# Kernel optimization log

Hardware: AMD Instinct MI355X
Metric: run time of the kernel (lower is better)

## Reference

```python
import jax, jax.numpy as jnp
from jax import lax
import numpy as np

KSIZE = 3
SOFTMAX_SCALE = 10.0
EPS = 1e-4  # escape_NaN in the original


def extract_patches(x, k):
    """x: [B,H,W,C] -> [B,H,W,k*k,C]; SAME zero padding, stride 1.
    Patch elements ordered (ky, kx) row-major, channels innermost, matching
    tf.image.extract_patches."""
    B, H, W, C = x.shape
    p = k // 2
    xp = jnp.pad(x, ((0, 0), (p, p), (p, p), (0, 0)))
    shifts = [xp[:, i:i + H, j:j + W, :] for i in range(k) for j in range(k)]
    return jnp.stack(shifts, axis=3)


def setup_inputs() -> dict:
    key = jax.random.key(0)
    k1, k2, k3 = jax.random.split(key, 3)
    B, H, W, C = 2, 64, 64, 128
    x1 = jax.random.normal(k1, (B, H, W, C), dtype=jnp.float32)
    x2 = jax.random.normal(k2, (B, H, W, C), dtype=jnp.float32)
    mask = jax.random.uniform(k3, (B, H, W, 1), dtype=jnp.float32)
    return {"x1": x1, "x2": x2, "mask": mask}


def reference(x1, x2, mask):
    # First call of the stateful layer: att_scores_prev is None, so the
    # mask-derived `mm` only updates internal state and does not affect y.
    # mask is already at x2's spatial size, so the bilinear resize is identity.
    B, H, W, C = x2.shape
    k = KSIZE
    L = H * W

    # Key patches from x2, L2-normalized per patch (the conv kernels).
    Pq = extract_patches(x2, k).reshape(B, L, k * k * C)  # [B, HW, k*k*C]
    norm = jnp.sqrt(jnp.sum(Pq * Pq, axis=-1, keepdims=True))
    Wn = Pq / jnp.maximum(norm, EPS)

    # conv2d(x2_i, wi_normed, SAME) == patches(x2_i) @ Wn_i^T  -> [B, HW, L]
    scores = jnp.einsum('bxq,blq->bxl', Pq, Wn).reshape(B, H, W, L)

    # tf.nn.avg_pool2d(., 3, 1, 'SAME') * 9 (TF excludes padding from count)
    sums = lax.reduce_window(scores, 0.0, lax.add, (1, 3, 3, 1), (1, 1, 1, 1), 'SAME')
    cnt = lax.reduce_window(jnp.ones((1, H, W, 1), scores.dtype), 0.0, lax.add,
                            (1, 3, 3, 1), (1, 1, 1, 1), 'SAME')
    pooled = sums / cnt * 9.0

    att = jax.nn.softmax(pooled * SOFTMAX_SCALE, axis=-1)  # [B, H, W, L]

    # Value patches from x1, arranged as conv kernels [k,k,C,L] per image.
    raw = extract_patches(x1, k).reshape(B, L, k, k, C).transpose(0, 2, 3, 4, 1)

    def tconv(a, kern):
        # tf.nn.conv2d_transpose(att, raw_wi, [1,H,W,C], strides=1, 'SAME')
        return lax.conv_transpose(a[None], kern, (1, 1), 'SAME',
                                  dimension_numbers=('NHWC', 'HWIO', 'NHWC'),
                                  transpose_kernel=True)[0]

    y = jax.vmap(tconv)(att, raw)  # [B, H, W, C]
    return y
```

## Files before the change

kernel.cpp:

```cpp
#include <hip/hip_runtime.h>
#include <hip/hip_bf16.h>
#include <math.h>


constexpr int Hh = 64;
constexpr int Ww = 64;
constexpr int CDIM = 128;
constexpr int LDIM = Hh * Ww;

typedef __attribute__((ext_vector_type(8))) short bf16x8;
typedef __attribute__((ext_vector_type(4))) float f32x4;
typedef __attribute__((ext_vector_type(4))) _Float16 f16x4;

__global__ __launch_bounds__(256)
void k_split(const float* __restrict__ X, __hip_bfloat16* __restrict__ Xh_,
             __hip_bfloat16* __restrict__ Xl_, size_t inStrideF, size_t wsStrideB) {
    const int z = blockIdx.z;
    const float* Xb = X + (size_t)z * inStrideF;
    __hip_bfloat16* Xh = (__hip_bfloat16*)((char*)Xh_ + (size_t)z * wsStrideB);
    __hip_bfloat16* Xl = (__hip_bfloat16*)((char*)Xl_ + (size_t)z * wsStrideB);
    const int i = (blockIdx.x * 256 + threadIdx.x) * 4;
    const float4 v = *(const float4*)(Xb + i);
    __hip_bfloat16 h[4], l[4];
    const float f[4] = {v.x, v.y, v.z, v.w};
    #pragma unroll
    for (int j = 0; j < 4; ++j) {
        h[j] = __float2bfloat16(f[j]);
        l[j] = __float2bfloat16(f[j] - __bfloat162float(h[j]));
    }
    *(ushort4*)(Xh + i) = *(ushort4*)h;
    *(ushort4*)(Xl + i) = *(ushort4*)l;
}

__global__ __launch_bounds__(256)
void k_pixnorm(const float* __restrict__ X2, float* __restrict__ pixn_,
               size_t inStrideF, size_t wsStrideB) {
    const int z = blockIdx.z;
    const float* Xb = X2 + (size_t)z * inStrideF;
    float* pixn = (float*)((char*)pixn_ + (size_t)z * wsStrideB);
    const int t = threadIdx.x;
    const int row = blockIdx.x * 64 + (t >> 2);
    const int seg = t & 3;
    const float* p = Xb + (size_t)row * CDIM + seg * 32;
    float s = 0.f;
    #pragma unroll
    for (int j = 0; j < 8; ++j) {
        const float4 v = *(const float4*)(p + 4 * j);
        s += v.x * v.x + v.y * v.y + v.z * v.z + v.w * v.w;
    }
    s += __shfl_xor(s, 1);
    s += __shfl_xor(s, 2);
    if (seg == 0) pixn[row] = s;
}

__global__ void k_invnorm(const float* __restrict__ pixn_, float* __restrict__ invn_,
                          size_t wsStrideB) {
    const int z = blockIdx.z;
    const float* pixn = (const float*)((const char*)pixn_ + (size_t)z * wsStrideB);
    float* invn = (float*)((char*)invn_ + (size_t)z * wsStrideB);
    const int l = blockIdx.x * 256 + threadIdx.x;
    const int ly = l >> 6, lx = l & 63;
    float s = 0.f;
    #pragma unroll
    for (int ty = -1; ty <= 1; ++ty)
        #pragma unroll
        for (int tx = -1; tx <= 1; ++tx) {
            if ((unsigned)(ly + ty) < 64u && (unsigned)(lx + tx) < 64u)
                s += pixn[l + ty * Ww + tx];
        }
    invn[l] = 1.0f / fmaxf(sqrtf(s), 1e-4f);
}

__global__ __launch_bounds__(256)
void k_gemm_d(const __hip_bfloat16* __restrict__ Xh_,
              const __hip_bfloat16* __restrict__ Xl_, _Float16* __restrict__ Ds_,
              size_t wsStrideB) {
    const int z = blockIdx.z;
    const __hip_bfloat16* Xh = (const __hip_bfloat16*)((const char*)Xh_ + (size_t)z * wsStrideB);
    const __hip_bfloat16* Xl = (const __hip_bfloat16*)((const char*)Xl_ + (size_t)z * wsStrideB);
    _Float16* Ds = (_Float16*)((char*)Ds_ + (size_t)z * wsStrideB);
    const int t = threadIdx.x;
    const int wave = t >> 6, lane = t & 63;
    const int quad = lane >> 4, l16 = lane & 15;
    const int bm = blockIdx.x * 128 + wave * 32;
    const int bn = blockIdx.y * 128;
    f32x4 acc[2][8] = {};
    for (int k0 = 0; k0 < CDIM; k0 += 32) {
        const int kq = k0 + quad * 8;
        bf16x8 ah[2], al[2], bh[8], bl[8];
        #pragma unroll
        for (int mi = 0; mi < 2; ++mi) {
            const size_t r = (size_t)(bm + mi * 16 + l16) * CDIM + kq;
            ah[mi] = *(const bf16x8*)(Xh + r);
            al[mi] = *(const bf16x8*)(Xl + r);
        }
        #pragma unroll
        for (int nf = 0; nf < 8; ++nf) {
            const size_t r = (size_t)(bn + nf * 16 + l16) * CDIM + kq;
            bh[nf] = *(const bf16x8*)(Xh + r);
            bl[nf] = *(const bf16x8*)(Xl + r);
        }
        #pragma unroll
        for (int mi = 0; mi < 2; ++mi)
            #pragma unroll
            for (int nf = 0; nf < 8; ++nf) {
                acc[mi][nf] = __builtin_amdgcn_mfma_f32_16x16x32_bf16(ah[mi], bh[nf], acc[mi][nf], 0, 0, 0);
                acc[mi][nf] = __builtin_amdgcn_mfma_f32_16x16x32_bf16(ah[mi], bl[nf], acc[mi][nf], 0, 0, 0);
                acc[mi][nf] = __builtin_amdgcn_mfma_f32_16x16x32_bf16(al[mi], bh[nf], acc[mi][nf], 0, 0, 0);
            }
    }
    #pragma unroll
    for (int mi = 0; mi < 2; ++mi)
        #pragma unroll
        for (int nf = 0; nf < 8; ++nf) {
            const int row = bm + mi * 16 + quad * 4;
            const int col = bn + nf * 16 + l16;
            #pragma unroll
            for (int r = 0; r < 4; ++r)
                Ds[(size_t)(row + r) * LDIM + ((col - row - r) & (LDIM - 1))] =
                    (_Float16)acc[mi][nf][r];
        }
}

__global__ __launch_bounds__(256)
void k_gdiag(const _Float16* __restrict__ Ds_, _Float16* __restrict__ G_,
             size_t wsStrideB) {
    const int z = blockIdx.z;
    const _Float16* Ds = (const _Float16*)((const char*)Ds_ + (size_t)z * wsStrideB);
    _Float16* G = (_Float16*)((char*)G_ + (size_t)z * wsStrideB);
    constexpr int T = 8;
    const int f = blockIdx.x + gridDim.x * blockIdx.y;
    const int swz = (f & 7) * 256 + (f >> 3);
    const int d0 = ((swz & 3) * 256 + threadIdx.x) * 4;
    const int x0 = (swz >> 2) * T;
    const int xyc = x0 >> 6;
    const int xxb = x0 & 63;
    float acc[T][4] = {};
    #pragma unroll
    for (int c = 0; c < 3; ++c) {
        const int bc = c * 64 - 65;
        const int ty = c - 1;
        if ((unsigned)(xyc + ty) >= 64u) continue;
        float w[T + 2][4];
        #pragma unroll
        for (int u = 0; u < T + 2; ++u) {
            const int r = x0 + bc + u;
            if ((unsigned)r < (unsigned)LDIM) {
                const f16x4 v = *(const f16x4*)(Ds + (size_t)r * LDIM + d0);
                w[u][0] = (float)v.x; w[u][1] = (float)v.y;
                w[u][2] = (float)v.z; w[u][3] = (float)v.w;
            } else {
                w[u][0] = w[u][1] = w[u][2] = w[u][3] = 0.f;
            }
        }
        #pragma unroll
        for (int i = 0; i < T; ++i) {
            const int px = xxb + i;
            const int p  = x0 + i;
            #pragma unroll
            for (int j = 0; j < 4; ++j) {
                const int l  = (p + d0 + j) & (LDIM - 1);
                const int ly = l >> 6, lx = l & 63;
                if ((unsigned)(ly + ty) < 64u) {
                    float s = acc[i][j];
                    if (px > 0 && lx > 0)   s += w[i][j];
                    s += w[i + 1][j];
                    if (px < 63 && lx < 63) s += w[i + 2][j];
                    acc[i][j] = s;
                }
            }
        }
    }
    #pragma unroll
    for (int i = 0; i < T; ++i) {
        const int x = x0 + i;
        const int l0i = (x + d0) & (LDIM - 1);
        union { _Float16 h[4]; unsigned short us[4]; unsigned int ui[2]; } cv;
        #pragma unroll
        for (int j = 0; j < 4; ++j) cv.h[j] = (_Float16)acc[i][j];
        unsigned short* bp = (unsigned short*)(G + (size_t)x * LDIM);
        if (l0i <= LDIM - 4) {
            if (!(l0i & 1)) {
                *(unsigned int*)(bp + l0i)     = cv.ui[0];
                *(unsigned int*)(bp + l0i + 2) = cv.ui[1];
            } else {
                bp[l0i] = cv.us[0];
                *(unsigned int*)(bp + l0i + 1) =
                    (unsigned int)cv.us[1] | ((unsigned int)cv.us[2] << 16);
                bp[l0i + 3] = cv.us[3];
            }
        } else {
            #pragma unroll
            for (int j = 0; j < 4; ++j)
                bp[(l0i + j) & (LDIM - 1)] = cv.us[j];
        }
    }
}

__global__ __launch_bounds__(256)
void k_pool_stats(const _Float16* __restrict__ G_, const float* __restrict__ invn_,
                  _Float16* __restrict__ Ps_, float* __restrict__ rowm_,
                  float* __restrict__ rowrz_, size_t wsStrideB) {
    const int z = blockIdx.z;
    const _Float16* G = (const _Float16*)((const char*)G_ + (size_t)z * wsStrideB);
    const float* invn = (const float*)((const char*)invn_ + (size_t)z * wsStrideB);
    _Float16* Ps = (_Float16*)((char*)Ps_ + (size_t)z * wsStrideB);
    float* rowm = (float*)((char*)rowm_ + (size_t)z * wsStrideB);
    float* rowrz = (float*)((char*)rowrz_ + (size_t)z * wsStrideB);
    constexpr int T = 8;
    const int f = blockIdx.x;
    const int swz = (f & 7) * 64 + (f >> 3);
    const int x0 = swz * T;
    const int t  = threadIdx.x;
    const int xyc = x0 >> 6;
    const int xxb = x0 & 63;
    const int cy = 1 + (xyc > 0) + (xyc < 63);
    float sc[T];
    #pragma unroll
    for (int i = 0; i < T; ++i) {
        const int xx = xxb + i;
        sc[i] = 90.0f / (float)(cy * (1 + (xx > 0) + (xx < 63)));
    }
    float m[T], Z[T];
    #pragma unroll
    for (int i = 0; i < T; ++i) { m[i] = -1e30f; Z[i] = 0.f; }

    for (int ch = 0; ch < 4; ++ch) {
        const int l0 = ch * 1024 + t * 4;
        const f32x4 inl = *(const f32x4*)(invn + l0);
        f32x4 acc[T];
        #pragma unroll
        for (int i = 0; i < T; ++i) acc[i] = (f32x4){0.f, 0.f, 0.f, 0.f};
        #pragma unroll
        for (int c = 0; c < 3; ++c) {
            const int bc = c * 64 - 65;
            const int ty = c - 1;
            if ((unsigned)(xyc + ty) >= 64u) continue;
            f32x4 w[T + 2];
            #pragma unroll
            for (int u = 0; u < T + 2; ++u) {
                const int r = x0 + bc + u;
                if ((unsigned)r < (unsigned)LDIM) {
                    const f16x4 v = *(const f16x4*)(G + (size_t)r * LDIM + l0);
                    w[u] = (f32x4){(float)v.x, (float)v.y, (float)v.z, (float)v.w};
                } else {
                    w[u] = (f32x4){0.f, 0.f, 0.f, 0.f};
                }
            }
            #pragma unroll
            for (int i = 0; i < T; ++i) {
                const int xx = xxb + i;
                if (xx > 0)  acc[i] += w[i];
                acc[i] += w[i + 1];
                if (xx < 63) acc[i] += w[i + 2];
            }
        }
        #pragma unroll
        for (int i = 0; i < T; ++i) {
            const f32x4 p = acc[i] * sc[i] * inl;
            const int x = x0 + i;
            const int c0 = (l0 - x) & (LDIM - 1);
            union { _Float16 h[4]; unsigned short us[4]; unsigned int ui[2]; } cv;
            float pr[4];
            #pragma unroll
            for (int j = 0; j < 4; ++j) {
                cv.h[j] = (_Float16)p[j];
                pr[j] = (float)cv.h[j];
            }
            unsigned short* bp = (unsigned short*)(Ps + (size_t)x * LDIM);
            if (c0 <= LDIM - 4) {
                if (!(c0 & 1)) {
                    *(unsigned int*)(bp + c0)     = cv.ui[0];
                    *(unsigned int*)(bp + c0 + 2) = cv.ui[1];
                } else {
                    bp[c0] = cv.us[0];
                    *(unsigned int*)(bp + c0 + 1) =
                        (unsigned int)cv.us[1] | ((unsigned int)cv.us[2] << 16);
                    bp[c0 + 3] = cv.us[3];
                }
            } else {
                #pragma unroll
                for (int j = 0; j < 4; ++j)
                    bp[(c0 + j) & (LDIM - 1)] = cv.us[j];
            }
            const float mx4 = fmaxf(fmaxf(pr[0], pr[1]), fmaxf(pr[2], pr[3]));
            const float nm = fmaxf(m[i], mx4);
            Z[i] = Z[i] * __expf(m[i] - nm)
                 + __expf(pr[0] - nm) + __expf(pr[1] - nm)
                 + __expf(pr[2] - nm) + __expf(pr[3] - nm);
            m[i] = nm;
        }
    }
    __shared__ float sm[256], sz[256];
    for (int i = 0; i < T; ++i) {
        __syncthreads();
        sm[t] = m[i]; sz[t] = Z[i];
        __syncthreads();
        for (int off = 128; off > 0; off >>= 1) {
            if (t < off) {
                const float m2 = sm[t + off], z2 = sz[t + off];
                const float nm = fmaxf(sm[t], m2);
                sz[t] = sz[t] * __expf(sm[t] - nm) + z2 * __expf(m2 - nm);
                sm[t] = nm;
            }
            __syncthreads();
        }
        if (t == 0) { rowm[x0 + i] = sm[0]; rowrz[x0 + i] = 1.0f / sz[0]; }
    }
}

__global__ __launch_bounds__(256)
void k_x1t(const float* __restrict__ X1, __hip_bfloat16* __restrict__ X1T_,
           size_t inStrideF, size_t wsStrideB) {
    const int z = blockIdx.z;
    const float* X1b = X1 + (size_t)z * inStrideF;
    __hip_bfloat16* X1T = (__hip_bfloat16*)((char*)X1T_ + (size_t)z * wsStrideB);
    __shared__ float tile[32][132];
    const int k0 = blockIdx.x * 32;
    const int t  = threadIdx.x;
    const int kr = t >> 3;
    const int c0 = (t & 7) * 16;
    #pragma unroll
    for (int j = 0; j < 4; ++j) {
        const float4 v = *(const float4*)(X1b + (size_t)(k0 + kr) * CDIM + c0 + 4 * j);
        tile[kr][c0 + 4 * j + 0] = v.x;
        tile[kr][c0 + 4 * j + 1] = v.y;
        tile[kr][c0 + 4 * j + 2] = v.z;
        tile[kr][c0 + 4 * j + 3] = v.w;
    }
    __syncthreads();
    const int c  = t >> 1;
    const int kh = (t & 1) * 16;
    __hip_bfloat16 outv[16];
    #pragma unroll
    for (int j = 0; j < 16; ++j)
        outv[j] = __float2bfloat16(tile[kh + j][c]);
    *(ushort4*)(X1T + (size_t)c * LDIM + k0 + kh)      = *(ushort4*)(outv);
    *(ushort4*)(X1T + (size_t)c * LDIM + k0 + kh + 4)  = *(ushort4*)(outv + 4);
    *(ushort4*)(X1T + (size_t)c * LDIM + k0 + kh + 8)  = *(ushort4*)(outv + 8);
    *(ushort4*)(X1T + (size_t)c * LDIM + k0 + kh + 12) = *(ushort4*)(outv + 12);
}

__global__ __launch_bounds__(256)
void k_att2(const _Float16* __restrict__ Ps_, const float* __restrict__ rowm_,
            const float* __restrict__ rowrz_, __hip_bfloat16* __restrict__ A2_,
            size_t wsStrideB) {
    const int z = blockIdx.z;
    const _Float16* Ps = (const _Float16*)((const char*)Ps_ + (size_t)z * wsStrideB);
    const float* rowm = (const float*)((const char*)rowm_ + (size_t)z * wsStrideB);
    const float* rowrz = (const float*)((const char*)rowrz_ + (size_t)z * wsStrideB);
    __hip_bfloat16* A2 = (__hip_bfloat16*)((char*)A2_ + (size_t)z * wsStrideB);
    constexpr int T = 8;
    const int f = blockIdx.x + gridDim.x * blockIdx.y;
    const int swz = (f & 7) * 256 + (f >> 3);
    const int d0 = ((swz & 3) * 256 + threadIdx.x) * 4;
    const int p0 = (swz >> 2) * T;
    const int pyc = p0 >> 6;
    const int pxb = p0 & 63;
    float acc[T][4] = {};
    #pragma unroll
    for (int c = 0; c < 3; ++c) {
        const int bc = c * 64 - 65;
        const int ty = c - 1;
        if ((unsigned)(pyc + ty) >= 64u) continue;
        float e[T + 2][4];
        #pragma unroll
        for (int u = 0; u < T + 2; ++u) {
            const int r = p0 + bc + u;
            if ((unsigned)r < (unsigned)LDIM) {
                const f16x4 w = *(const f16x4*)(Ps + (size_t)r * LDIM + d0);
                const float mr = rowm[r], rzr = rowrz[r];
                e[u][0] = __expf((float)w.x - mr) * rzr;
                e[u][1] = __expf((float)w.y - mr) * rzr;
                e[u][2] = __expf((float)w.z - mr) * rzr;
                e[u][3] = __expf((float)w.w - mr) * rzr;
            } else {
                e[u][0] = e[u][1] = e[u][2] = e[u][3] = 0.f;
            }
        }
        #pragma unroll
        for (int i = 0; i < T; ++i) {
            const int px = pxb + i;
            const int p  = p0 + i;
            #pragma unroll
            for (int j = 0; j < 4; ++j) {
                const int q  = (p + d0 + j) & (LDIM - 1);
                const int qy = q >> 6, qx = q & 63;
                if ((unsigned)(qy + ty) < 64u) {
                    float s = acc[i][j];
                    if (px > 0 && qx > 0)   s += e[i][j];
                    s += e[i + 1][j];
                    if (px < 63 && qx < 63) s += e[i + 2][j];
                    acc[i][j] = s;
                }
            }
        }
    }
    #pragma unroll
    for (int i = 0; i < T; ++i) {
        const int p = p0 + i;
        const int q0i = (p + d0) & (LDIM - 1);
        union { __hip_bfloat16 h[4]; unsigned short us[4]; unsigned int ui[2]; } cv;
        #pragma unroll
        for (int j = 0; j < 4; ++j) cv.h[j] = __float2bfloat16(acc[i][j]);
        unsigned short* bp = (unsigned short*)(A2 + (size_t)p * LDIM);
        if (q0i <= LDIM - 4) {
            if (!(q0i & 1)) {
                *(unsigned int*)(bp + q0i)     = cv.ui[0];
                *(unsigned int*)(bp + q0i + 2) = cv.ui[1];
            } else {
                bp[q0i] = cv.us[0];
                *(unsigned int*)(bp + q0i + 1) =
                    (unsigned int)cv.us[1] | ((unsigned int)cv.us[2] << 16);
                bp[q0i + 3] = cv.us[3];
            }
        } else {
            #pragma unroll
            for (int j = 0; j < 4; ++j)
                bp[(q0i + j) & (LDIM - 1)] = cv.us[j];
        }
    }
}

__global__ __launch_bounds__(256)
void k_gemm_y(const __hip_bfloat16* __restrict__ A2b_,
              const __hip_bfloat16* __restrict__ X1T_, float* __restrict__ Y_,
              size_t wsStrideB, size_t outStrideF) {
    const int z = blockIdx.z;
    const __hip_bfloat16* A2b = (const __hip_bfloat16*)((const char*)A2b_ + (size_t)z * wsStrideB);
    const __hip_bfloat16* X1T = (const __hip_bfloat16*)((const char*)X1T_ + (size_t)z * wsStrideB);
    float* Y = Y_ + (size_t)z * outStrideF;
    const int t = threadIdx.x;
    const int wave = t >> 6, lane = t & 63;
    const int quad = lane >> 4, l16 = lane & 15;
    const int bm = blockIdx.x * 128 + wave * 32;
    const int kc = blockIdx.y * 512;
    f32x4 acc[2][8] = {};
    for (int ks = 0; ks < 512; ks += 32) {
        const int kq = kc + ks + quad * 8;
        bf16x8 a[2], b[8];
        #pragma unroll
        for (int mi = 0; mi < 2; ++mi)
            a[mi] = *(const bf16x8*)(A2b + (size_t)(bm + mi * 16 + l16) * LDIM + kq);
        #pragma unroll
        for (int nf = 0; nf < 8; ++nf)
            b[nf] = *(const bf16x8*)(X1T + (size_t)(nf * 16 + l16) * LDIM + kq);
        #pragma unroll
        for (int mi = 0; mi < 2; ++mi)
            #pragma unroll
            for (int nf = 0; nf < 8; ++nf)
                acc[mi][nf] = __builtin_amdgcn_mfma_f32_16x16x32_bf16(a[mi], b[nf], acc[mi][nf], 0, 0, 0);
    }
    #pragma unroll
    for (int mi = 0; mi < 2; ++mi)
        #pragma unroll
        for (int nf = 0; nf < 8; ++nf)
            #pragma unroll
            for (int r = 0; r < 4; ++r)
                atomicAdd(Y + (size_t)(bm + mi * 16 + quad * 4 + r) * CDIM + nf * 16 + l16,
                          acc[mi][nf][r]);
}

extern "C" void kernel_launch(void* const* d_in, const int* in_sizes, int n_in,
                              void* d_out, int out_size, void* d_ws, size_t ws_size,
                              hipStream_t stream) {
    const float* x1 = (const float*)d_in[0];
    const float* x2 = (const float*)d_in[1];
    float* out = (float*)d_out;

    const size_t MATB = (size_t)LDIM * LDIM * sizeof(float);
    const size_t HMATB = MATB / 2;
    const size_t SMALLB = (size_t)64 * 1024;
    const size_t SLICE = HMATB + HMATB + (size_t)LDIM * CDIM * sizeof(__hip_bfloat16) + SMALLB;

    const int B = in_sizes[0] / (LDIM * CDIM);
    const size_t inStrideF = (size_t)LDIM * CDIM;
    const bool concurrent = ((size_t)B * SLICE <= ws_size);

    (void)hipMemsetAsync(d_out, 0, (size_t)out_size * sizeof(float), stream);

    const int NB = concurrent ? B : 1;
    const int NL = concurrent ? 1 : B;
    const size_t wsStrideB = concurrent ? SLICE : 0;

    for (int b = 0; b < NL; ++b) {
        char* ws = (char*)d_ws;
        _Float16* Dsh = (_Float16*)ws;
        _Float16* Psh = (_Float16*)ws;
        char* buf2c = ws + HMATB;
        _Float16* Gh = (_Float16*)buf2c;
        __hip_bfloat16* X2h = (__hip_bfloat16*)buf2c;
        __hip_bfloat16* X2l = (__hip_bfloat16*)(buf2c + (size_t)LDIM * CDIM * 2);
        __hip_bfloat16* A2b = (__hip_bfloat16*)buf2c;
        __hip_bfloat16* X1T = (__hip_bfloat16*)(buf2c + HMATB);
        float* invn  = (float*)(ws + HMATB + HMATB + (size_t)LDIM * CDIM * sizeof(__hip_bfloat16));
        float* rowm  = invn + LDIM;
        float* rowrz = rowm + LDIM;
        float* pixn  = rowrz + LDIM;

        const float* X2b_ = x2 + (size_t)b * inStrideF;
        const float* X1b_ = x1 + (size_t)b * inStrideF;
        float* Yb = out + (size_t)b * inStrideF;
        const size_t inS = concurrent ? inStrideF : 0;
        const size_t outS = concurrent ? inStrideF : 0;

        k_split     <<<dim3(LDIM * CDIM / 1024, 1, NB), 256, 0, stream>>>(X2b_, X2h, X2l, inS, wsStrideB);
        k_pixnorm   <<<dim3(LDIM / 64, 1, NB), 256, 0, stream>>>(X2b_, pixn, inS, wsStrideB);
        k_invnorm   <<<dim3(LDIM / 256, 1, NB), 256, 0, stream>>>(pixn, invn, wsStrideB);
        k_gemm_d    <<<dim3(LDIM / 128, LDIM / 128, NB), 256, 0, stream>>>(X2h, X2l, Dsh, wsStrideB);
        k_gdiag     <<<dim3(LDIM / 1024, LDIM / 8, NB), 256, 0, stream>>>(Dsh, Gh, wsStrideB);
        k_pool_stats<<<dim3(LDIM / 8, 1, NB), 256, 0, stream>>>(Gh, invn, Psh, rowm, rowrz, wsStrideB);
        k_x1t       <<<dim3(LDIM / 32, 1, NB), 256, 0, stream>>>(X1b_, X1T, inS, wsStrideB);
        k_att2      <<<dim3(LDIM / 1024, LDIM / 8, NB), 256, 0, stream>>>(Psh, rowm, rowrz, A2b, wsStrideB);
        k_gemm_y    <<<dim3(LDIM / 128, 8, NB), 256, 0, stream>>>(A2b, X1T, Yb, wsStrideB, outS);
    }
}
```

Before: 399.4 us.

## Split pool_stats over column chunks and reduce row stats with wave shuffles

k_pool_stats now launches four blocks per 8-row tile, one per 1024-column chunk, instead of looping over the chunks inside a single block. Each block writes partial max and sum-of-exponentials to a scratch buffer, and a new k_stats_combine kernel merges them into the row max and reciprocal sum. The shared-memory tree reduction with many barriers is replaced by wave shuffle reductions plus a single barrier. This raises parallelism and cuts synchronisation, at the cost of an extra kernel launch and a scratch buffer that aliases the X1T region, which is written only after the combine step.

```diff
diff --git a/kernel.cpp b/kernel.cpp
--- a/kernel.cpp
+++ b/kernel.cpp
@@ -199,19 +199,20 @@
 
 __global__ __launch_bounds__(256)
 void k_pool_stats(const _Float16* __restrict__ G_, const float* __restrict__ invn_,
-                  _Float16* __restrict__ Ps_, float* __restrict__ rowm_,
-                  float* __restrict__ rowrz_, size_t wsStrideB) {
+                  _Float16* __restrict__ Ps_, float* __restrict__ pmz_,
+                  size_t wsStrideB) {
     const int z = blockIdx.z;
     const _Float16* G = (const _Float16*)((const char*)G_ + (size_t)z * wsStrideB);
     const float* invn = (const float*)((const char*)invn_ + (size_t)z * wsStrideB);
     _Float16* Ps = (_Float16*)((char*)Ps_ + (size_t)z * wsStrideB);
-    float* rowm = (float*)((char*)rowm_ + (size_t)z * wsStrideB);
-    float* rowrz = (float*)((char*)rowrz_ + (size_t)z * wsStrideB);
+    float* pmz = (float*)((char*)pmz_ + (size_t)z * wsStrideB);
     constexpr int T = 8;
     const int f = blockIdx.x;
     const int swz = (f & 7) * 64 + (f >> 3);
     const int x0 = swz * T;
+    const int ch = blockIdx.y;
     const int t  = threadIdx.x;
+    const int wave = t >> 6, lane = t & 63;
     const int xyc = x0 >> 6;
     const int xxb = x0 & 63;
     const int cy = 1 + (xyc > 0) + (xyc < 63);
@@ -222,91 +223,117 @@
         sc[i] = 90.0f / (float)(cy * (1 + (xx > 0) + (xx < 63)));
     }
     float m[T], Z[T];
-    #pragma unroll
-    for (int i = 0; i < T; ++i) { m[i] = -1e30f; Z[i] = 0.f; }
-
-    for (int ch = 0; ch < 4; ++ch) {
-        const int l0 = ch * 1024 + t * 4;
-        const f32x4 inl = *(const f32x4*)(invn + l0);
-        f32x4 acc[T];
-        #pragma unroll
-        for (int i = 0; i < T; ++i) acc[i] = (f32x4){0.f, 0.f, 0.f, 0.f};
-        #pragma unroll
-        for (int c = 0; c < 3; ++c) {
-            const int bc = c * 64 - 65;
-            const int ty = c - 1;
-            if ((unsigned)(xyc + ty) >= 64u) continue;
-            f32x4 w[T + 2];
-            #pragma unroll
-            for (int u = 0; u < T + 2; ++u) {
-                const int r = x0 + bc + u;
-                if ((unsigned)r < (unsigned)LDIM) {
-                    const f16x4 v = *(const f16x4*)(G + (size_t)r * LDIM + l0);
-                    w[u] = (f32x4){(float)v.x, (float)v.y, (float)v.z, (float)v.w};
-                } else {
-                    w[u] = (f32x4){0.f, 0.f, 0.f, 0.f};
-                }
-            }
-            #pragma unroll
-            for (int i = 0; i < T; ++i) {
-                const int xx = xxb + i;
-                if (xx > 0)  acc[i] += w[i];
-                acc[i] += w[i + 1];
-                if (xx < 63) acc[i] += w[i + 2];
+
+    const int l0 = ch * 1024 + t * 4;
+    const f32x4 inl = *(const f32x4*)(invn + l0);
+    f32x4 acc[T];
+    #pragma unroll
+    for (int i = 0; i < T; ++i) acc[i] = (f32x4){0.f, 0.f, 0.f, 0.f};
+    #pragma unroll
+    for (int c = 0; c < 3; ++c) {
+        const int bc = c * 64 - 65;
+        const int ty = c - 1;
+        if ((unsigned)(xyc + ty) >= 64u) continue;
+        f32x4 w[T + 2];
+        #pragma unroll
+        for (int u = 0; u < T + 2; ++u) {
+            const int r = x0 + bc + u;
+            if ((unsigned)r < (unsigned)LDIM) {
+                const f16x4 v = *(const f16x4*)(G + (size_t)r * LDIM + l0);
+                w[u] = (f32x4){(float)v.x, (float)v.y, (float)v.z, (float)v.w};
+            } else {
+                w[u] = (f32x4){0.f, 0.f, 0.f, 0.f};
             }
         }
         #pragma unroll
         for (int i = 0; i < T; ++i) {
-            const f32x4 p = acc[i] * sc[i] * inl;
-            const int x = x0 + i;
-            const int c0 = (l0 - x) & (LDIM - 1);
-            union { _Float16 h[4]; unsigned short us[4]; unsigned int ui[2]; } cv;
-            float pr[4];
-            #pragma unroll
-            for (int j = 0; j < 4; ++j) {
-                cv.h[j] = (_Float16)p[j];
-                pr[j] = (float)cv.h[j];
-            }
-            unsigned short* bp = (unsigned short*)(Ps + (size_t)x * LDIM);
-            if (c0 <= LDIM - 4) {
-                if (!(c0 & 1)) {
-                    *(unsigned int*)(bp + c0)     = cv.ui[0];
-                    *(unsigned int*)(bp + c0 + 2) = cv.ui[1];
-                } else {
-                    bp[c0] = cv.us[0];
-                    *(unsigned int*)(bp + c0 + 1) =
-                        (unsigned int)cv.us[1] | ((unsigned int)cv.us[2] << 16);
-                    bp[c0 + 3] = cv.us[3];
-                }
+            const int xx = xxb + i;
+            if (xx > 0)  acc[i] += w[i];
+            acc[i] += w[i + 1];
+            if (xx < 63) acc[i] += w[i + 2];
+        }
+    }
+    #pragma unroll
+    for (int i = 0; i < T; ++i) {
+        const f32x4 p = acc[i] * sc[i] * inl;
+        const int x = x0 + i;
+        const int c0 = (l0 - x) & (LDIM - 1);
+        union { _Float16 h[4]; unsigned short us[4]; unsigned int ui[2]; } cv;
+        float pr[4];
+        #pragma unroll
+        for (int j = 0; j < 4; ++j) {
+            cv.h[j] = (_Float16)p[j];
+            pr[j] = (float)cv.h[j];
+        }
+        unsigned short* bp = (unsigned short*)(Ps + (size_t)x * LDIM);
+        if (c0 <= LDIM - 4) {
+            if (!(c0 & 1)) {
+                *(unsigned int*)(bp + c0)     = cv.ui[0];
+                *(unsigned int*)(bp + c0 + 2) = cv.ui[1];
             } else {
-                #pragma unroll
-                for (int j = 0; j < 4; ++j)
-                    bp[(c0 + j) & (LDIM - 1)] = cv.us[j];
-            }
-            const float mx4 = fmaxf(fmaxf(pr[0], pr[1]), fmaxf(pr[2], pr[3]));
-            const float nm = fmaxf(m[i], mx4);
-            Z[i] = Z[i] * __expf(m[i] - nm)
-                 + __expf(pr[0] - nm) + __expf(pr[1] - nm)
-                 + __expf(pr[2] - nm) + __expf(pr[3] - nm);
-            m[i] = nm;
-        }
-    }
-    __shared__ float sm[256], sz[256];
+                bp[c0] = cv.us[0];
+                *(unsigned int*)(bp + c0 + 1) =
+                    (unsigned int)cv.us[1] | ((unsigned int)cv.us[2] << 16);
+                bp[c0 + 3] = cv.us[3];
+            }
+        } else {
+            #pragma unroll
+            for (int j = 0; j < 4; ++j)
+                bp[(c0 + j) & (LDIM - 1)] = cv.us[j];
+        }
+        const float mx = fmaxf(fmaxf(pr[0], pr[1]), fmaxf(pr[2], pr[3]));
+        m[i] = mx;
+        Z[i] = __expf(pr[0] - mx) + __expf(pr[1] - mx)
+             + __expf(pr[2] - mx) + __expf(pr[3] - mx);
+    }
+    __shared__ float sm[4][T], sz[4][T];
+    #pragma unroll
     for (int i = 0; i < T; ++i) {
-        __syncthreads();
-        sm[t] = m[i]; sz[t] = Z[i];
-        __syncthreads();
-        for (int off = 128; off > 0; off >>= 1) {
-            if (t < off) {
-                const float m2 = sm[t + off], z2 = sz[t + off];
-                const float nm = fmaxf(sm[t], m2);
-                sz[t] = sz[t] * __expf(sm[t] - nm) + z2 * __expf(m2 - nm);
-                sm[t] = nm;
-            }
-            __syncthreads();
-        }
-        if (t == 0) { rowm[x0 + i] = sm[0]; rowrz[x0 + i] = 1.0f / sz[0]; }
-    }
+        float mi = m[i], zi = Z[i];
+        #pragma unroll
+        for (int s = 1; s < 64; s <<= 1) {
+            const float m2 = __shfl_xor(mi, s);
+            const float z2 = __shfl_xor(zi, s);
+            const float nm = fmaxf(mi, m2);
+            zi = zi * __expf(mi - nm) + z2 * __expf(m2 - nm);
+            mi = nm;
+        }
+        if (lane == 0) { sm[wave][i] = mi; sz[wave][i] = zi; }
+    }
+    __syncthreads();
+    if (t < T) {
+        float mi = sm[0][t], zi = sz[0][t];
+        #pragma unroll
+        for (int wv = 1; wv < 4; ++wv) {
+            const float m2 = sm[wv][t], z2 = sz[wv][t];
+            const float nm = fmaxf(mi, m2);
+            zi = zi * __expf(mi - nm) + z2 * __expf(m2 - nm);
+            mi = nm;
+        }
+        pmz[(size_t)ch * LDIM + x0 + t] = mi;
+        pmz[(size_t)(4 + ch) * LDIM + x0 + t] = zi;
+    }
+}
+
+__global__ __launch_bounds__(256)
+void k_stats_combine(const float* __restrict__ pmz_, float* __restrict__ rowm_,
+                     float* __restrict__ rowrz_, size_t wsStrideB) {
+    const int z = blockIdx.z;
+    const float* pmz = (const float*)((const char*)pmz_ + (size_t)z * wsStrideB);
+    float* rowm = (float*)((char*)rowm_ + (size_t)z * wsStrideB);
+    float* rowrz = (float*)((char*)rowrz_ + (size_t)z * wsStrideB);
+    const int l = blockIdx.x * 256 + threadIdx.x;
+    float mi = pmz[l], zi = pmz[(size_t)4 * LDIM + l];
+    #pragma unroll
+    for (int ch = 1; ch < 4; ++ch) {
+        const float m2 = pmz[(size_t)ch * LDIM + l];
+        const float z2 = pmz[(size_t)(4 + ch) * LDIM + l];
+        const float nm = fmaxf(mi, m2);
+        zi = zi * __expf(mi - nm) + z2 * __expf(m2 - nm);
+        mi = nm;
+    }
+    rowm[l] = mi;
+    rowrz[l] = 1.0f / zi;
 }
 
 __global__ __launch_bounds__(256)
@@ -493,6 +520,7 @@
         __hip_bfloat16* X2l = (__hip_bfloat16*)(buf2c + (size_t)LDIM * CDIM * 2);
         __hip_bfloat16* A2b = (__hip_bfloat16*)buf2c;
         __hip_bfloat16* X1T = (__hip_bfloat16*)(buf2c + HMATB);
+        float* pmz = (float*)(buf2c + HMATB);
         float* invn  = (float*)(ws + HMATB + HMATB + (size_t)LDIM * CDIM * sizeof(__hip_bfloat16));
         float* rowm  = invn + LDIM;
         float* rowrz = rowm + LDIM;
@@ -504,14 +532,15 @@
         const size_t inS = concurrent ? inStrideF : 0;
         const size_t outS = concurrent ? inStrideF : 0;
 
-        k_split     <<<dim3(LDIM * CDIM / 1024, 1, NB), 256, 0, stream>>>(X2b_, X2h, X2l, inS, wsStrideB);
-        k_pixnorm   <<<dim3(LDIM / 64, 1, NB), 256, 0, stream>>>(X2b_, pixn, inS, wsStrideB);
-        k_invnorm   <<<dim3(LDIM / 256, 1, NB), 256, 0, stream>>>(pixn, invn, wsStrideB);
-        k_gemm_d    <<<dim3(LDIM / 128, LDIM / 128, NB), 256, 0, stream>>>(X2h, X2l, Dsh, wsStrideB);
-        k_gdiag     <<<dim3(LDIM / 1024, LDIM / 8, NB), 256, 0, stream>>>(Dsh, Gh, wsStrideB);
-        k_pool_stats<<<dim3(LDIM / 8, 1, NB), 256, 0, stream>>>(Gh, invn, Psh, rowm, rowrz, wsStrideB);
-        k_x1t       <<<dim3(LDIM / 32, 1, NB), 256, 0, stream>>>(X1b_, X1T, inS, wsStrideB);
-        k_att2      <<<dim3(LDIM / 1024, LDIM / 8, NB), 256, 0, stream>>>(Psh, rowm, rowrz, A2b, wsStrideB);
-        k_gemm_y    <<<dim3(LDIM / 128, 8, NB), 256, 0, stream>>>(A2b, X1T, Yb, wsStrideB, outS);
-    }
-}
+        k_split        <<<dim3(LDIM * CDIM / 1024, 1, NB), 256, 0, stream>>>(X2b_, X2h, X2l, inS, wsStrideB);
+        k_pixnorm      <<<dim3(LDIM / 64, 1, NB), 256, 0, stream>>>(X2b_, pixn, inS, wsStrideB);
+        k_invnorm      <<<dim3(LDIM / 256, 1, NB), 256, 0, stream>>>(pixn, invn, wsStrideB);
+        k_gemm_d       <<<dim3(LDIM / 128, LDIM / 128, NB), 256, 0, stream>>>(X2h, X2l, Dsh, wsStrideB);
+        k_gdiag        <<<dim3(LDIM / 1024, LDIM / 8, NB), 256, 0, stream>>>(Dsh, Gh, wsStrideB);
+        k_pool_stats   <<<dim3(LDIM / 8, 4, NB), 256, 0, stream>>>(Gh, invn, Psh, pmz, wsStrideB);
+        k_stats_combine<<<dim3(LDIM / 256, 1, NB), 256, 0, stream>>>(pmz, rowm, rowrz, wsStrideB);
+        k_x1t          <<<dim3(LDIM / 32, 1, NB), 256, 0, stream>>>(X1b_, X1T, inS, wsStrideB);
+        k_att2         <<<dim3(LDIM / 1024, LDIM / 8, NB), 256, 0, stream>>>(Psh, rowm, rowrz, A2b, wsStrideB);
+        k_gemm_y       <<<dim3(LDIM / 128, 8, NB), 256, 0, stream>>>(A2b, X1T, Yb, wsStrideB, outS);
+    }
+}
```

Measured after the change: 361.8 us. 1.1x faster.
